# Performance work log

Hardware: AMD Instinct MI355X
Metric: run time of the kernel (lower is better)

The kernel has to match this reference:

```python
import jax, jax.numpy as jnp
import numpy as np

NUM_CLASSES = 10
THRESHOLD = 2e-4
ENT_COEF = 2e-4
COS_EPS = 1e-8
LOG_EPS = 1e-12


def setup_inputs() -> dict:
    key = jax.random.key(0)
    k1, k2, k3 = jax.random.split(key, 3)
    B, C, H, W = 256, 256, 8, 8
    M, F = 2000, C * H * W
    z = jax.random.normal(k1, (B, C, H, W), dtype=jnp.float32)
    labels = jax.random.randint(k2, (B,), 0, NUM_CLASSES)
    # kaiming-uniform-like init for the memory table
    bound = float(np.sqrt(6.0 / F))
    memory = jax.random.uniform(k3, (M, F), dtype=jnp.float32, minval=-bound, maxval=bound)
    return {"z": z, "labels": labels, "memory": memory}


def _shrink_l1norm(w):
    # hardshrink (strict |x| > lambda) then L1 renormalize along memories
    w = jnp.where(jnp.abs(w) > THRESHOLD, w, jnp.zeros_like(w))
    return w / jnp.sum(jnp.abs(w), axis=1, keepdims=True)


def _entropy_loss(w):
    return ENT_COEF * jnp.sum(-w * jnp.log(w + LOG_EPS))


def reference(z, labels, memory):
    B, C, H, W = z.shape
    M, F = memory.shape
    zf = z.reshape(B, F)
    # cosine similarity without materializing (B, M, F): dot / max(||z||*||m||, eps)
    nz = jnp.linalg.norm(zf, axis=1)              # (B,)
    nm = jnp.linalg.norm(memory, axis=1)          # (M,)
    logit = (zf @ memory.T) / jnp.maximum(nz[:, None] * nm[None, :], COS_EPS)  # (B, M)
    mem_weight = jax.nn.softmax(logit, axis=1)
    # per-class masks: memory slots are partitioned contiguously per class
    mem_per_class = M // NUM_CLASSES
    cls_of_mem = jnp.arange(M) // mem_per_class   # (M,)
    m1 = (cls_of_mem[None, :] == labels[:, None]).astype(mem_weight.dtype)  # target mask
    m2 = 1.0 - m1
    w_t = _shrink_l1norm(mem_weight * m1)
    w_nt = _shrink_l1norm(mem_weight * m2)
    z_hat_target = (w_t @ memory).reshape(B, C, H, W)
    z_hat_non_target = (w_nt @ memory).reshape(B, C, H, W)
    return (z_hat_target, z_hat_non_target, _entropy_loss(w_t), _entropy_loss(w_nt))
```

## Files before the change

kernel.cpp:

```cpp
#include <hip/hip_runtime.h>
#include <math.h>

#define BATCH 256
#define FDIM 16384
#define MSLOTS 2000
#define MPAD 2048
#define NCLS 10
#define MPC 200

static constexpr float THRESH = 2e-4f;
static constexpr float ENTC   = 2e-4f;
static constexpr float CEPS   = 1e-8f;
static constexpr float LEPS   = 1e-12f;

using bf16x8 = __attribute__((ext_vector_type(8))) short;
using f32x4  = __attribute__((ext_vector_type(4))) float;
using us8    = __attribute__((ext_vector_type(8))) unsigned short;

__device__ __forceinline__ unsigned short f2bf(float f) {
  unsigned u = __float_as_uint(f);
  unsigned r = u + 0x7fffu + ((u >> 16) & 1u);
  return (unsigned short)(r >> 16);
}

__device__ __forceinline__ void gload_lds16(const unsigned short* g, unsigned short* l) {
  __builtin_amdgcn_global_load_lds(
      (const __attribute__((address_space(1))) void*)g,
      (__attribute__((address_space(3))) void*)l, 16, 0, 0);
}

__device__ __forceinline__ float waveReduceSum(float v) {
#pragma unroll
  for (int o = 32; o > 0; o >>= 1) v += __shfl_xor(v, o);
  return v;
}
__device__ __forceinline__ float waveReduceMax(float v) {
#pragma unroll
  for (int o = 32; o > 0; o >>= 1) v = fmaxf(v, __shfl_xor(v, o));
  return v;
}


__global__ __launch_bounds__(256) void convert_z_kernel(const float* __restrict__ z,
                                                        unsigned short* __restrict__ zb,
                                                        float* __restrict__ nz) {
  const int b = blockIdx.x, tid = threadIdx.x;
  const float4* zr = reinterpret_cast<const float4*>(z + (size_t)b * FDIM);
  unsigned short* ob = zb + (size_t)b * FDIM;
  float s = 0.f;
  for (int i = tid; i < FDIM / 4; i += 256) {
    float4 v = zr[i];
    s = fmaf(v.x, v.x, fmaf(v.y, v.y, fmaf(v.z, v.z, fmaf(v.w, v.w, s))));
    ushort4 o;
    o.x = f2bf(v.x); o.y = f2bf(v.y); o.z = f2bf(v.z); o.w = f2bf(v.w);
    *reinterpret_cast<ushort4*>(&ob[i * 4]) = o;
  }
  s = waveReduceSum(s);
  __shared__ float red[4];
  if ((tid & 63) == 0) red[tid >> 6] = s;
  __syncthreads();
  if (tid == 0) nz[b] = sqrtf(red[0] + red[1] + red[2] + red[3]);
}

__global__ __launch_bounds__(256) void convert_mem_kernel(const float* __restrict__ mem,
                                                          unsigned short* __restrict__ mb,
                                                          float* __restrict__ nm) {
  const int r = blockIdx.x, tid = threadIdx.x;
  unsigned short* ob = mb + (size_t)r * FDIM;
  if (r >= MSLOTS) {
    us8 zed = (us8)0;
    for (int i = tid; i < FDIM / 8; i += 256)
      *reinterpret_cast<us8*>(&ob[i * 8]) = zed;
    if (tid == 0) nm[r] = 1.0f;
    return;
  }
  const float4* xr = reinterpret_cast<const float4*>(mem + (size_t)r * FDIM);
  float s = 0.f;
  for (int i = tid; i < FDIM / 4; i += 256) {
    float4 v = xr[i];
    s = fmaf(v.x, v.x, fmaf(v.y, v.y, fmaf(v.z, v.z, fmaf(v.w, v.w, s))));
    ushort4 o;
    o.x = f2bf(v.x); o.y = f2bf(v.y); o.z = f2bf(v.z); o.w = f2bf(v.w);
    *reinterpret_cast<ushort4*>(&ob[i * 4]) = o;
  }
  s = waveReduceSum(s);
  __shared__ float red[4];
  if ((tid & 63) == 0) red[tid >> 6] = s;
  __syncthreads();
  if (tid == 0) nm[r] = sqrtf(red[0] + red[1] + red[2] + red[3]);
}

__global__ __launch_bounds__(256) void transpose_kernel(const unsigned short* __restrict__ src,
                                                        unsigned short* __restrict__ dst) {
  __shared__ unsigned short t[64][72];
  const int f0 = blockIdx.x * 64, m0 = blockIdx.y * 64;
  const int tid = threadIdx.x;
#pragma unroll
  for (int it = 0; it < 2; ++it) {
    int r = (tid >> 3) + it * 32, c8 = tid & 7;
    us8 v = *reinterpret_cast<const us8*>(&src[(size_t)(m0 + r) * FDIM + f0 + c8 * 8]);
    *reinterpret_cast<us8*>(&t[r][c8 * 8]) = v;
  }
  __syncthreads();
#pragma unroll
  for (int it = 0; it < 2; ++it) {
    int rf = (tid >> 3) + it * 32, c8 = tid & 7;
    us8 v;
#pragma unroll
    for (int j = 0; j < 8; ++j) v[j] = t[c8 * 8 + j][rf];
    *reinterpret_cast<us8*>(&dst[(size_t)(f0 + rf) * MPAD + m0 + c8 * 8]) = v;
  }
}

#define G1_BM 128
#define G1_BN 64
#define G1_BK 64
#define SPLITK 8
#define KCHUNK (FDIM / SPLITK)

__global__ __launch_bounds__(256, 2) void gemm1_mfma(const unsigned short* __restrict__ zb,
                                                     const unsigned short* __restrict__ mb,
                                                     float* __restrict__ part) {
  __shared__ unsigned short As[G1_BM * G1_BK];
  __shared__ unsigned short Bs[G1_BN * G1_BK];
  const int tid = threadIdx.x;
  const int lane = tid & 63, wid = tid >> 6;
  const int bn0 = blockIdx.x * G1_BN;
  const int bm0 = blockIdx.y * G1_BM;
  const int kbase = blockIdx.z * KCHUNK;
  const int wr = wid >> 1, wc = wid & 1;
  const int l8 = lane >> 3, l7 = lane & 7;
  const int r16 = lane & 15, klane = lane >> 4;

  f32x4 acc[4][2] = {};

  for (int kt = 0; kt < KCHUNK; kt += G1_BK) {
    const int kg = kbase + kt;
#pragma unroll
    for (int it = 0; it < 4; ++it) {
      int c = wid + it * 4;
      int r = c * 8 + l8;
      int src = (l7 ^ (r & 7)) << 3;
      gload_lds16(&zb[(size_t)(bm0 + r) * FDIM + kg + src], &As[c * 512]);
    }
#pragma unroll
    for (int it = 0; it < 2; ++it) {
      int c = wid + it * 4;
      int r = c * 8 + l8;
      int src = (l7 ^ (r & 7)) << 3;
      gload_lds16(&mb[(size_t)(bn0 + r) * FDIM + kg + src], &Bs[c * 512]);
    }
    __syncthreads();
#pragma unroll
    for (int s = 0; s < 2; ++s) {
      bf16x8 a[4], bb[2];
#pragma unroll
      for (int i = 0; i < 4; ++i) {
        int r = wr * 64 + i * 16 + r16;
        int p = (s * 4 + klane) ^ (r & 7);
        a[i] = *reinterpret_cast<const bf16x8*>(&As[r * 64 + p * 8]);
      }
#pragma unroll
      for (int j = 0; j < 2; ++j) {
        int r = wc * 32 + j * 16 + r16;
        int p = (s * 4 + klane) ^ (r & 7);
        bb[j] = *reinterpret_cast<const bf16x8*>(&Bs[r * 64 + p * 8]);
      }
#pragma unroll
      for (int i = 0; i < 4; ++i)
#pragma unroll
        for (int j = 0; j < 2; ++j)
          acc[i][j] = __builtin_amdgcn_mfma_f32_16x16x32_bf16(a[i], bb[j], acc[i][j], 0, 0, 0);
    }
    __syncthreads();
  }
  const int rgrp = lane >> 4;
  float* pbase = part + (size_t)blockIdx.z * BATCH * MPAD;
#pragma unroll
  for (int i = 0; i < 4; ++i)
#pragma unroll
    for (int j = 0; j < 2; ++j)
#pragma unroll
      for (int rg = 0; rg < 4; ++rg) {
        int row = bm0 + wr * 64 + i * 16 + rgrp * 4 + rg;
        int col = bn0 + wc * 32 + j * 16 + r16;
        pbase[(size_t)row * MPAD + col] = acc[i][j][rg];
      }
}

__global__ __launch_bounds__(256) void softmax2_kernel(const float* __restrict__ part,
                                                       const float* __restrict__ nzv,
                                                       const float* __restrict__ nmv,
                                                       const int* __restrict__ labels,
                                                       unsigned short* __restrict__ wt,
                                                       unsigned short* __restrict__ wn,
                                                       float* __restrict__ ent) {
  const int b = blockIdx.x, tid = threadIdx.x;
  __shared__ float sh[MSLOTS];
  __shared__ float red[4], red2[4];
  const float nzb = nzv[b];
  float mx = -3.4e38f;
  for (int m = tid; m < MSLOTS; m += 256) {
    float s = 0.f;
#pragma unroll
    for (int sp = 0; sp < SPLITK; ++sp)
      s += part[((size_t)sp * BATCH + b) * MPAD + m];
    float v = s / fmaxf(nzb * nmv[m], CEPS);
    sh[m] = v; mx = fmaxf(mx, v);
  }
  mx = waveReduceMax(mx);
  if ((tid & 63) == 0) red[tid >> 6] = mx;
  __syncthreads();
  mx = fmaxf(fmaxf(red[0], red[1]), fmaxf(red[2], red[3]));
  __syncthreads();

  float s = 0.f;
  for (int m = tid; m < MSLOTS; m += 256) {
    float e = expf(sh[m] - mx); sh[m] = e; s += e;
  }
  s = waveReduceSum(s);
  if ((tid & 63) == 0) red[tid >> 6] = s;
  __syncthreads();
  s = red[0] + red[1] + red[2] + red[3];
  __syncthreads();

  const float inv = 1.f / s;
  const int c = labels[b];
  const int t0 = c * MPC, t1 = t0 + MPC;
  float st = 0.f, sn = 0.f;
  for (int m = tid; m < MSLOTS; m += 256) {
    float w = sh[m] * inv;
    float k = (w > THRESH) ? w : 0.f;
    sh[m] = k;
    bool tgt = (m >= t0) && (m < t1);
    st += tgt ? k : 0.f;
    sn += tgt ? 0.f : k;
  }
  st = waveReduceSum(st); sn = waveReduceSum(sn);
  if ((tid & 63) == 0) { red[tid >> 6] = st; red2[tid >> 6] = sn; }
  __syncthreads();
  st = red[0] + red[1] + red[2] + red[3];
  sn = red2[0] + red2[1] + red2[2] + red2[3];
  __syncthreads();

  const float rt = 1.f / st, rn = 1.f / sn;
  float et = 0.f, en = 0.f;
  unsigned short* wtr = wt + (size_t)b * MPAD;
  unsigned short* wnr = wn + (size_t)b * MPAD;
  for (int m = tid; m < MPAD; m += 256) {
    float a = 0.f, cn = 0.f;
    if (m < MSLOTS) {
      float k = sh[m];
      bool tgt = (m >= t0) && (m < t1);
      a  = tgt ? k * rt : 0.f;
      cn = tgt ? 0.f : k * rn;
      et -= a  * logf(a  + LEPS);
      en -= cn * logf(cn + LEPS);
    }
    wtr[m] = f2bf(a);
    wnr[m] = f2bf(cn);
  }
  et = waveReduceSum(et); en = waveReduceSum(en);
  if ((tid & 63) == 0) { red[tid >> 6] = et; red2[tid >> 6] = en; }
  __syncthreads();
  if (tid == 0) {
    ent[b]         = red[0] + red[1] + red[2] + red[3];
    ent[BATCH + b] = red2[0] + red2[1] + red2[2] + red2[3];
  }
}

#define G2_BM 128
#define G2_BN 128
#define G2_BK 64

__global__ __launch_bounds__(512, 2) void gemm23_mfma(const unsigned short* __restrict__ wt,
                                                      const unsigned short* __restrict__ wn,
                                                      const unsigned short* __restrict__ mt,
                                                      float* __restrict__ out) {
  __shared__ unsigned short At[G2_BM * G2_BK];
  __shared__ unsigned short An[G2_BM * G2_BK];
  __shared__ unsigned short Bs[G2_BN * G2_BK];
  const int tid = threadIdx.x, lane = tid & 63, wid = tid >> 6;
  const int bn0 = blockIdx.x * G2_BN;
  const int bm0 = blockIdx.y * G2_BM;
  const int wr = wid >> 2, wc = wid & 3;
  const int l8 = lane >> 3, l7 = lane & 7;
  const int r16 = lane & 15, klane = lane >> 4;

  f32x4 acct[4][2] = {}, accn[4][2] = {};

  for (int k0 = 0; k0 < MPAD; k0 += G2_BK) {
#pragma unroll
    for (int it = 0; it < 2; ++it) {
      int c = wid + it * 8;
      int r = c * 8 + l8;
      int src = (l7 ^ (r & 7)) << 3;
      gload_lds16(&wt[(size_t)(bm0 + r) * MPAD + k0 + src], &At[c * 512]);
      gload_lds16(&wn[(size_t)(bm0 + r) * MPAD + k0 + src], &An[c * 512]);
      gload_lds16(&mt[(size_t)(bn0 + r) * MPAD + k0 + src], &Bs[c * 512]);
    }
    __syncthreads();
#pragma unroll
    for (int s = 0; s < 2; ++s) {
      bf16x8 at[4], an[4], bb[2];
#pragma unroll
      for (int i = 0; i < 4; ++i) {
        int r = wr * 64 + i * 16 + r16;
        int p = (s * 4 + klane) ^ (r & 7);
        at[i] = *reinterpret_cast<const bf16x8*>(&At[r * 64 + p * 8]);
        an[i] = *reinterpret_cast<const bf16x8*>(&An[r * 64 + p * 8]);
      }
#pragma unroll
      for (int j = 0; j < 2; ++j) {
        int r = wc * 32 + j * 16 + r16;
        int p = (s * 4 + klane) ^ (r & 7);
        bb[j] = *reinterpret_cast<const bf16x8*>(&Bs[r * 64 + p * 8]);
      }
#pragma unroll
      for (int i = 0; i < 4; ++i)
#pragma unroll
        for (int j = 0; j < 2; ++j) {
          acct[i][j] = __builtin_amdgcn_mfma_f32_16x16x32_bf16(at[i], bb[j], acct[i][j], 0, 0, 0);
          accn[i][j] = __builtin_amdgcn_mfma_f32_16x16x32_bf16(an[i], bb[j], accn[i][j], 0, 0, 0);
        }
    }
    __syncthreads();
  }
  float* outn = out + (size_t)BATCH * FDIM;
  const int rgrp = lane >> 4;
#pragma unroll
  for (int i = 0; i < 4; ++i)
#pragma unroll
    for (int j = 0; j < 2; ++j)
#pragma unroll
      for (int rg = 0; rg < 4; ++rg) {
        size_t off = (size_t)(bm0 + wr * 64 + i * 16 + rgrp * 4 + rg) * FDIM
                   + bn0 + wc * 32 + j * 16 + r16;
        out[off]  = acct[i][j][rg];
        outn[off] = accn[i][j][rg];
      }
}

__global__ __launch_bounds__(256) void entreduce_kernel(const float* __restrict__ ent,
                                                        float* __restrict__ out) {
  const int tid = threadIdx.x;
  float v = ent[tid];
  float u = ent[BATCH + tid];
  v = waveReduceSum(v); u = waveReduceSum(u);
  __shared__ float r1[4], r2[4];
  if ((tid & 63) == 0) { r1[tid >> 6] = v; r2[tid >> 6] = u; }
  __syncthreads();
  if (tid == 0) {
    out[(size_t)2 * BATCH * FDIM]     = ENTC * (r1[0] + r1[1] + r1[2] + r1[3]);
    out[(size_t)2 * BATCH * FDIM + 1] = ENTC * (r2[0] + r2[1] + r2[2] + r2[3]);
  }
}

#define NM_OFF    0
#define NZ_OFF    2048
#define LOGIT_OFF 4096
#define WT_OFF    (LOGIT_OFF + 512000)
#define WNT_OFF   (WT_OFF + 512000)
#define ENT_OFF   (WNT_OFF + 512000)

__global__ __launch_bounds__(256) void rownorm_kernel(const float* __restrict__ x,
                                                      float* __restrict__ out, int cols) {
  const int r = blockIdx.x;
  const float4* xr = reinterpret_cast<const float4*>(x) + (size_t)r * (cols >> 2);
  const int n4 = cols >> 2;
  float s = 0.f;
  for (int i = threadIdx.x; i < n4; i += 256) {
    float4 v = xr[i];
    s = fmaf(v.x, v.x, s); s = fmaf(v.y, v.y, s);
    s = fmaf(v.z, v.z, s); s = fmaf(v.w, v.w, s);
  }
  s = waveReduceSum(s);
  __shared__ float red[4];
  if ((threadIdx.x & 63) == 0) red[threadIdx.x >> 6] = s;
  __syncthreads();
  if (threadIdx.x == 0) out[r] = sqrtf(red[0] + red[1] + red[2] + red[3]);
}

#define O1_BM 64
#define O1_BN 32
#define O1_BK 64
__global__ __launch_bounds__(256) void gemm1_kernel(const float* __restrict__ z,
                                                    const float* __restrict__ mem,
                                                    const float* __restrict__ nzv,
                                                    const float* __restrict__ nmv,
                                                    float* __restrict__ logit) {
  __shared__ float As[O1_BK][O1_BM];
  __shared__ float Bs[O1_BK][O1_BN];
  const int tid = threadIdx.x;
  const int bm0 = blockIdx.y * O1_BM;
  const int bn0 = blockIdx.x * O1_BN;
  const int tm = tid >> 4, tn = tid & 15;
  float acc[4][2] = {};
  for (int k0 = 0; k0 < FDIM; k0 += O1_BK) {
#pragma unroll
    for (int it = 0; it < 4; ++it) {
      int i = tid + it * 256;
      int row = i >> 4, c4 = i & 15;
      float4 v = *reinterpret_cast<const float4*>(&z[(size_t)(bm0 + row) * FDIM + k0 + c4 * 4]);
      As[c4 * 4 + 0][row] = v.x; As[c4 * 4 + 1][row] = v.y;
      As[c4 * 4 + 2][row] = v.z; As[c4 * 4 + 3][row] = v.w;
    }
#pragma unroll
    for (int it = 0; it < 2; ++it) {
      int i = tid + it * 256;
      int row = i >> 4, c4 = i & 15;
      int gm = bn0 + row;
      float4 v = make_float4(0.f, 0.f, 0.f, 0.f);
      if (gm < MSLOTS)
        v = *reinterpret_cast<const float4*>(&mem[(size_t)gm * FDIM + k0 + c4 * 4]);
      Bs[c4 * 4 + 0][row] = v.x; Bs[c4 * 4 + 1][row] = v.y;
      Bs[c4 * 4 + 2][row] = v.z; Bs[c4 * 4 + 3][row] = v.w;
    }
    __syncthreads();
#pragma unroll
    for (int kk = 0; kk < O1_BK; ++kk) {
      const float* ap = &As[kk][tm * 4];
      const float* bp = &Bs[kk][tn * 2];
      float a0 = ap[0], a1 = ap[1], a2 = ap[2], a3 = ap[3];
      float b0 = bp[0], b1 = bp[1];
      acc[0][0] = fmaf(a0, b0, acc[0][0]); acc[0][1] = fmaf(a0, b1, acc[0][1]);
      acc[1][0] = fmaf(a1, b0, acc[1][0]); acc[1][1] = fmaf(a1, b1, acc[1][1]);
      acc[2][0] = fmaf(a2, b0, acc[2][0]); acc[2][1] = fmaf(a2, b1, acc[2][1]);
      acc[3][0] = fmaf(a3, b0, acc[3][0]); acc[3][1] = fmaf(a3, b1, acc[3][1]);
    }
    __syncthreads();
  }
  float nzr[4];
#pragma unroll
  for (int i = 0; i < 4; ++i) nzr[i] = nzv[bm0 + tm * 4 + i];
#pragma unroll
  for (int j = 0; j < 2; ++j) {
    int col = bn0 + tn * 2 + j;
    if (col < MSLOTS) {
      float nmr = nmv[col];
#pragma unroll
      for (int i = 0; i < 4; ++i)
        logit[(size_t)(bm0 + tm * 4 + i) * MSLOTS + col] = acc[i][j] / fmaxf(nzr[i] * nmr, CEPS);
    }
  }
}

__global__ __launch_bounds__(256) void softmax_kernel(const float* __restrict__ logit,
                                                      const int* __restrict__ labels,
                                                      float* __restrict__ wt,
                                                      float* __restrict__ wnt,
                                                      float* __restrict__ ent) {
  const int b = blockIdx.x;
  const int tid = threadIdx.x;
  __shared__ float sh[MSLOTS];
  __shared__ float red[4], red2[4];
  const float* lrow = logit + (size_t)b * MSLOTS;
  float mx = -3.4e38f;
  for (int m = tid; m < MSLOTS; m += 256) {
    float v = lrow[m]; sh[m] = v; mx = fmaxf(mx, v);
  }
  mx = waveReduceMax(mx);
  if ((tid & 63) == 0) red[tid >> 6] = mx;
  __syncthreads();
  mx = fmaxf(fmaxf(red[0], red[1]), fmaxf(red[2], red[3]));
  __syncthreads();
  float s = 0.f;
  for (int m = tid; m < MSLOTS; m += 256) {
    float e = expf(sh[m] - mx); sh[m] = e; s += e;
  }
  s = waveReduceSum(s);
  if ((tid & 63) == 0) red[tid >> 6] = s;
  __syncthreads();
  s = red[0] + red[1] + red[2] + red[3];
  __syncthreads();
  const float inv = 1.f / s;
  const int c = labels[b];
  const int t0 = c * MPC, t1 = t0 + MPC;
  float st = 0.f, sn = 0.f;
  for (int m = tid; m < MSLOTS; m += 256) {
    float w = sh[m] * inv;
    float k = (w > THRESH) ? w : 0.f;
    sh[m] = k;
    bool tgt = (m >= t0) && (m < t1);
    st += tgt ? k : 0.f;
    sn += tgt ? 0.f : k;
  }
  st = waveReduceSum(st); sn = waveReduceSum(sn);
  if ((tid & 63) == 0) { red[tid >> 6] = st; red2[tid >> 6] = sn; }
  __syncthreads();
  st = red[0] + red[1] + red[2] + red[3];
  sn = red2[0] + red2[1] + red2[2] + red2[3];
  __syncthreads();
  const float rt = 1.f / st, rn = 1.f / sn;
  float et = 0.f, en = 0.f;
  float* wtr = wt + (size_t)b * MSLOTS;
  float* wnr = wnt + (size_t)b * MSLOTS;
  for (int m = tid; m < MSLOTS; m += 256) {
    float k = sh[m];
    bool tgt = (m >= t0) && (m < t1);
    float a  = tgt ? k * rt : 0.f;
    float cn = tgt ? 0.f : k * rn;
    wtr[m] = a;
    wnr[m] = cn;
    et -= a  * logf(a  + LEPS);
    en -= cn * logf(cn + LEPS);
  }
  et = waveReduceSum(et); en = waveReduceSum(en);
  if ((tid & 63) == 0) { red[tid >> 6] = et; red2[tid >> 6] = en; }
  __syncthreads();
  if (tid == 0) {
    ent[b]         = red[0] + red[1] + red[2] + red[3];
    ent[BATCH + b] = red2[0] + red2[1] + red2[2] + red2[3];
  }
}

#define O2_BM 64
#define O2_BN 64
#define O2_BK 32
__global__ __launch_bounds__(256) void gemm23_kernel(const float* __restrict__ wt,
                                                     const float* __restrict__ wnt,
                                                     const float* __restrict__ mem,
                                                     float* __restrict__ out) {
  __shared__ float Wts[O2_BK][O2_BM];
  __shared__ float Wns[O2_BK][O2_BM];
  __shared__ float Ms[O2_BK][O2_BN];
  const int tid = threadIdx.x;
  const int bm0 = blockIdx.y * O2_BM;
  const int bn0 = blockIdx.x * O2_BN;
  const int tm = tid >> 4, tn = tid & 15;
  float at[4][4] = {}, an[4][4] = {};
  for (int k0 = 0; k0 < MSLOTS; k0 += O2_BK) {
#pragma unroll
    for (int it = 0; it < 2; ++it) {
      int i = tid + it * 256;
      int row = i >> 3, c4 = i & 7;
      int gk = k0 + c4 * 4;
      float4 vt = make_float4(0.f, 0.f, 0.f, 0.f), vn = vt;
      if (gk < MSLOTS) {
        vt = *reinterpret_cast<const float4*>(&wt [(size_t)(bm0 + row) * MSLOTS + gk]);
        vn = *reinterpret_cast<const float4*>(&wnt[(size_t)(bm0 + row) * MSLOTS + gk]);
      }
      Wts[c4 * 4 + 0][row] = vt.x; Wts[c4 * 4 + 1][row] = vt.y;
      Wts[c4 * 4 + 2][row] = vt.z; Wts[c4 * 4 + 3][row] = vt.w;
      Wns[c4 * 4 + 0][row] = vn.x; Wns[c4 * 4 + 1][row] = vn.y;
      Wns[c4 * 4 + 2][row] = vn.z; Wns[c4 * 4 + 3][row] = vn.w;
    }
#pragma unroll
    for (int it = 0; it < 2; ++it) {
      int i = tid + it * 256;
      int row = i >> 4, c4 = i & 15;
      int gk = k0 + row;
      float4 v = make_float4(0.f, 0.f, 0.f, 0.f);
      if (gk < MSLOTS)
        v = *reinterpret_cast<const float4*>(&mem[(size_t)gk * FDIM + bn0 + c4 * 4]);
      *reinterpret_cast<float4*>(&Ms[row][c4 * 4]) = v;
    }
    __syncthreads();
#pragma unroll
    for (int kk = 0; kk < O2_BK; ++kk) {
      const float* tp = &Wts[kk][tm * 4];
      const float* np = &Wns[kk][tm * 4];
      const float* bp = &Ms[kk][tn * 4];
      float b0 = bp[0], b1 = bp[1], b2 = bp[2], b3 = bp[3];
#pragma unroll
      for (int i = 0; i < 4; ++i) {
        float a = tp[i], cn = np[i];
        at[i][0] = fmaf(a,  b0, at[i][0]); at[i][1] = fmaf(a,  b1, at[i][1]);
        at[i][2] = fmaf(a,  b2, at[i][2]); at[i][3] = fmaf(a,  b3, at[i][3]);
        an[i][0] = fmaf(cn, b0, an[i][0]); an[i][1] = fmaf(cn, b1, an[i][1]);
        an[i][2] = fmaf(cn, b2, an[i][2]); an[i][3] = fmaf(cn, b3, an[i][3]);
      }
    }
    __syncthreads();
  }
  float* outt = out;
  float* outn = out + (size_t)BATCH * FDIM;
#pragma unroll
  for (int i = 0; i < 4; ++i) {
    size_t off = (size_t)(bm0 + tm * 4 + i) * FDIM + bn0 + tn * 4;
    *reinterpret_cast<float4*>(&outt[off]) = make_float4(at[i][0], at[i][1], at[i][2], at[i][3]);
    *reinterpret_cast<float4*>(&outn[off]) = make_float4(an[i][0], an[i][1], an[i][2], an[i][3]);
  }
}

extern "C" void kernel_launch(void* const* d_in, const int* in_sizes, int n_in,
                              void* d_out, int out_size, void* d_ws, size_t ws_size,
                              hipStream_t stream) {
  const float* z      = (const float*)d_in[0];
  const int*   labels = (const int*)d_in[1];
  const float* mem    = (const float*)d_in[2];
  float* out = (float*)d_out;
  char*  wsb = (char*)d_ws;

  constexpr size_t NM_B  = 0;
  constexpr size_t NZ_B  = 8192;
  constexpr size_t ZB_B  = 16384;
  constexpr size_t MB_B  = ZB_B + (size_t)BATCH * FDIM * 2;
  constexpr size_t MT_B  = MB_B + (size_t)MPAD * FDIM * 2;
  constexpr size_t WTB_B = MT_B + (size_t)FDIM * MPAD * 2;
  constexpr size_t WNB_B = WTB_B + (size_t)BATCH * MPAD * 2;
  constexpr size_t PART_B = WNB_B + (size_t)BATCH * MPAD * 2;
  constexpr size_t ENT_B = PART_B + (size_t)SPLITK * BATCH * MPAD * 4;
  constexpr size_t NEED  = ENT_B + 2048;

  if (ws_size >= NEED) {
    float* nm = (float*)(wsb + NM_B);
    float* nz = (float*)(wsb + NZ_B);
    unsigned short* zb = (unsigned short*)(wsb + ZB_B);
    unsigned short* mb = (unsigned short*)(wsb + MB_B);
    unsigned short* mt = (unsigned short*)(wsb + MT_B);
    unsigned short* wt = (unsigned short*)(wsb + WTB_B);
    unsigned short* wn = (unsigned short*)(wsb + WNB_B);
    float* part = (float*)(wsb + PART_B);
    float* ent  = (float*)(wsb + ENT_B);

    convert_z_kernel<<<BATCH, 256, 0, stream>>>(z, zb, nz);
    convert_mem_kernel<<<MPAD, 256, 0, stream>>>(mem, mb, nm);
    transpose_kernel<<<dim3(FDIM / 64, MPAD / 64), 256, 0, stream>>>(mb, mt);
    gemm1_mfma<<<dim3(MPAD / G1_BN, BATCH / G1_BM, SPLITK), 256, 0, stream>>>(zb, mb, part);
    softmax2_kernel<<<BATCH, 256, 0, stream>>>(part, nz, nm, labels, wt, wn, ent);
    gemm23_mfma<<<dim3(FDIM / G2_BN, BATCH / G2_BM), 512, 0, stream>>>(wt, wn, mt, out);
    entreduce_kernel<<<1, 256, 0, stream>>>(ent, out);
  } else {
    float* ws    = (float*)d_ws;
    float* nm    = ws + NM_OFF;
    float* nzv   = ws + NZ_OFF;
    float* logit = ws + LOGIT_OFF;
    float* wt    = ws + WT_OFF;
    float* wnt   = ws + WNT_OFF;
    float* ent   = ws + ENT_OFF;

    rownorm_kernel<<<MSLOTS, 256, 0, stream>>>(mem, nm, FDIM);
    rownorm_kernel<<<BATCH, 256, 0, stream>>>(z, nzv, FDIM);
    gemm1_kernel<<<dim3((MSLOTS + O1_BN - 1) / O1_BN, BATCH / O1_BM), 256, 0, stream>>>(
        z, mem, nzv, nm, logit);
    softmax_kernel<<<BATCH, 256, 0, stream>>>(logit, labels, wt, wnt, ent);
    gemm23_kernel<<<dim3(FDIM / O2_BN, BATCH / O2_BM), 256, 0, stream>>>(wt, wnt, mem, out);
    entreduce_kernel<<<1, 256, 0, stream>>>(ent, out);
  }
}
```

Baseline: 168.5 us.

## Fuse bf16 conversion, row norms and transpose into one tiled kernel

Replaces the separate z/mem conversion kernels and the bf16 transpose kernel with a single 2D-tiled kernel. Each 64x64 tile is read from fp32, converted, and written as row-major bf16, and for memory tiles also transposed. Partial squared norms are written per tile and finished by a small reduction kernel. This avoids re-reading the bf16 memory copy for the transpose and cuts launches. In exchange, norms are now computed from bf16-rounded values and padding rows get a zero norm.

Measured after the change: 149.4 us. 1.13x faster.

```diff
diff --git a/kernel.cpp b/kernel.cpp
--- a/kernel.cpp
+++ b/kernel.cpp
@@ -7,6 +7,7 @@
 #define MPAD 2048
 #define NCLS 10
 #define MPC 200
+#define NFB (FDIM / 64)
 
 static constexpr float THRESH = 2e-4f;
 static constexpr float ENTC   = 2e-4f;
@@ -22,6 +23,9 @@
   unsigned r = u + 0x7fffu + ((u >> 16) & 1u);
   return (unsigned short)(r >> 16);
 }
+__device__ __forceinline__ float bf2f(unsigned short b) {
+  return __uint_as_float(((unsigned)b) << 16);
+}
 
 __device__ __forceinline__ void gload_lds16(const unsigned short* g, unsigned short* l) {
   __builtin_amdgcn_global_load_lds(
@@ -41,74 +45,83 @@
 }
 
 
-__global__ __launch_bounds__(256) void convert_z_kernel(const float* __restrict__ z,
-                                                        unsigned short* __restrict__ zb,
-                                                        float* __restrict__ nz) {
-  const int b = blockIdx.x, tid = threadIdx.x;
-  const float4* zr = reinterpret_cast<const float4*>(z + (size_t)b * FDIM);
-  unsigned short* ob = zb + (size_t)b * FDIM;
-  float s = 0.f;
-  for (int i = tid; i < FDIM / 4; i += 256) {
-    float4 v = zr[i];
-    s = fmaf(v.x, v.x, fmaf(v.y, v.y, fmaf(v.z, v.z, fmaf(v.w, v.w, s))));
+__global__ __launch_bounds__(256) void convert_all_kernel(
+    const float* __restrict__ z, const float* __restrict__ mem,
+    unsigned short* __restrict__ zb, unsigned short* __restrict__ mb,
+    unsigned short* __restrict__ mt, float* __restrict__ npart) {
+  __shared__ unsigned short t[64][72];
+  __shared__ float rsum[64][4];
+  const int tid = threadIdx.x;
+  const int f0 = blockIdx.x * 64;
+  const int yt = blockIdx.y;
+  const bool isMem = (yt < MPAD / 64);
+  const int r0 = isMem ? yt * 64 : (yt - MPAD / 64) * 64;
+  const float* src = isMem ? mem : z;
+
+#pragma unroll
+  for (int it = 0; it < 4; ++it) {
+    int i = tid + it * 256;
+    int r = i >> 4, c4 = i & 15;
+    int gr = r0 + r;
+    float4 v = make_float4(0.f, 0.f, 0.f, 0.f);
+    if (!isMem || gr < MSLOTS)
+      v = *reinterpret_cast<const float4*>(&src[(size_t)gr * FDIM + f0 + c4 * 4]);
     ushort4 o;
     o.x = f2bf(v.x); o.y = f2bf(v.y); o.z = f2bf(v.z); o.w = f2bf(v.w);
-    *reinterpret_cast<ushort4*>(&ob[i * 4]) = o;
-  }
+    *reinterpret_cast<ushort4*>(&t[r][c4 * 4]) = o;
+  }
+  __syncthreads();
+  {
+    int r = tid & 63, q = tid >> 6;
+    float s = 0.f;
+#pragma unroll
+    for (int c = 0; c < 16; ++c) {
+      float val = bf2f(t[r][q * 16 + c]);
+      s = fmaf(val, val, s);
+    }
+    rsum[r][q] = s;
+  }
+  __syncthreads();
+  if (tid < 64) {
+    float s = rsum[tid][0] + rsum[tid][1] + rsum[tid][2] + rsum[tid][3];
+    int row = isMem ? (r0 + tid) : (MPAD + r0 + tid);
+    npart[(size_t)row * NFB + blockIdx.x] = s;
+  }
+  unsigned short* dst = isMem ? mb : zb;
+#pragma unroll
+  for (int it = 0; it < 2; ++it) {
+    int i = tid + it * 256;
+    int r = i >> 3, c8 = i & 7;
+    us8 v = *reinterpret_cast<const us8*>(&t[r][c8 * 8]);
+    *reinterpret_cast<us8*>(&dst[(size_t)(r0 + r) * FDIM + f0 + c8 * 8]) = v;
+  }
+  if (isMem) {
+#pragma unroll
+    for (int it = 0; it < 2; ++it) {
+      int i = tid + it * 256;
+      int fr = i >> 3, c8 = i & 7;
+      us8 v;
+#pragma unroll
+      for (int j = 0; j < 8; ++j) v[j] = t[c8 * 8 + j][fr];
+      *reinterpret_cast<us8*>(&mt[(size_t)(f0 + fr) * MPAD + r0 + c8 * 8]) = v;
+    }
+  }
+}
+
+__global__ __launch_bounds__(64) void normfin_kernel(const float* __restrict__ npart,
+                                                     float* __restrict__ nm,
+                                                     float* __restrict__ nz) {
+  const int row = blockIdx.x;
+  const int lane = threadIdx.x;
+  const float* p = npart + (size_t)row * NFB;
+  float s = 0.f;
+#pragma unroll
+  for (int k = 0; k < NFB / 64; ++k) s += p[lane + k * 64];
   s = waveReduceSum(s);
-  __shared__ float red[4];
-  if ((tid & 63) == 0) red[tid >> 6] = s;
-  __syncthreads();
-  if (tid == 0) nz[b] = sqrtf(red[0] + red[1] + red[2] + red[3]);
-}
-
-__global__ __launch_bounds__(256) void convert_mem_kernel(const float* __restrict__ mem,
-                                                          unsigned short* __restrict__ mb,
-                                                          float* __restrict__ nm) {
-  const int r = blockIdx.x, tid = threadIdx.x;
-  unsigned short* ob = mb + (size_t)r * FDIM;
-  if (r >= MSLOTS) {
-    us8 zed = (us8)0;
-    for (int i = tid; i < FDIM / 8; i += 256)
-      *reinterpret_cast<us8*>(&ob[i * 8]) = zed;
-    if (tid == 0) nm[r] = 1.0f;
-    return;
-  }
-  const float4* xr = reinterpret_cast<const float4*>(mem + (size_t)r * FDIM);
-  float s = 0.f;
-  for (int i = tid; i < FDIM / 4; i += 256) {
-    float4 v = xr[i];
-    s = fmaf(v.x, v.x, fmaf(v.y, v.y, fmaf(v.z, v.z, fmaf(v.w, v.w, s))));
-    ushort4 o;
-    o.x = f2bf(v.x); o.y = f2bf(v.y); o.z = f2bf(v.z); o.w = f2bf(v.w);
-    *reinterpret_cast<ushort4*>(&ob[i * 4]) = o;
-  }
-  s = waveReduceSum(s);
-  __shared__ float red[4];
-  if ((tid & 63) == 0) red[tid >> 6] = s;
-  __syncthreads();
-  if (tid == 0) nm[r] = sqrtf(red[0] + red[1] + red[2] + red[3]);
-}
-
-__global__ __launch_bounds__(256) void transpose_kernel(const unsigned short* __restrict__ src,
-                                                        unsigned short* __restrict__ dst) {
-  __shared__ unsigned short t[64][72];
-  const int f0 = blockIdx.x * 64, m0 = blockIdx.y * 64;
-  const int tid = threadIdx.x;
-#pragma unroll
-  for (int it = 0; it < 2; ++it) {
-    int r = (tid >> 3) + it * 32, c8 = tid & 7;
-    us8 v = *reinterpret_cast<const us8*>(&src[(size_t)(m0 + r) * FDIM + f0 + c8 * 8]);
-    *reinterpret_cast<us8*>(&t[r][c8 * 8]) = v;
-  }
-  __syncthreads();
-#pragma unroll
-  for (int it = 0; it < 2; ++it) {
-    int rf = (tid >> 3) + it * 32, c8 = tid & 7;
-    us8 v;
-#pragma unroll
-    for (int j = 0; j < 8; ++j) v[j] = t[c8 * 8 + j][rf];
-    *reinterpret_cast<us8*>(&dst[(size_t)(f0 + rf) * MPAD + m0 + c8 * 8]) = v;
+  if (lane == 0) {
+    float v = sqrtf(s);
+    if (row < MPAD) nm[row] = v;
+    else            nz[row - MPAD] = v;
   }
 }
 
@@ -592,16 +605,17 @@
   float* out = (float*)d_out;
   char*  wsb = (char*)d_ws;
 
-  constexpr size_t NM_B  = 0;
-  constexpr size_t NZ_B  = 8192;
-  constexpr size_t ZB_B  = 16384;
-  constexpr size_t MB_B  = ZB_B + (size_t)BATCH * FDIM * 2;
-  constexpr size_t MT_B  = MB_B + (size_t)MPAD * FDIM * 2;
-  constexpr size_t WTB_B = MT_B + (size_t)FDIM * MPAD * 2;
-  constexpr size_t WNB_B = WTB_B + (size_t)BATCH * MPAD * 2;
-  constexpr size_t PART_B = WNB_B + (size_t)BATCH * MPAD * 2;
-  constexpr size_t ENT_B = PART_B + (size_t)SPLITK * BATCH * MPAD * 4;
-  constexpr size_t NEED  = ENT_B + 2048;
+  constexpr size_t NM_B   = 0;
+  constexpr size_t NZ_B   = 8192;
+  constexpr size_t ZB_B   = 16384;
+  constexpr size_t MB_B   = ZB_B + (size_t)BATCH * FDIM * 2;
+  constexpr size_t MT_B   = MB_B + (size_t)MPAD * FDIM * 2;
+  constexpr size_t WTB_B  = MT_B + (size_t)FDIM * MPAD * 2;
+  constexpr size_t WNB_B  = WTB_B + (size_t)BATCH * MPAD * 2;
+  constexpr size_t NP_B   = WNB_B + (size_t)BATCH * MPAD * 2;
+  constexpr size_t PART_B = NP_B + (size_t)(MPAD + BATCH) * NFB * 4;
+  constexpr size_t ENT_B  = PART_B + (size_t)SPLITK * BATCH * MPAD * 4;
+  constexpr size_t NEED   = ENT_B + 2048;
 
   if (ws_size >= NEED) {
     float* nm = (float*)(wsb + NM_B);
@@ -611,12 +625,13 @@
     unsigned short* mt = (unsigned short*)(wsb + MT_B);
     unsigned short* wt = (unsigned short*)(wsb + WTB_B);
     unsigned short* wn = (unsigned short*)(wsb + WNB_B);
-    float* part = (float*)(wsb + PART_B);
-    float* ent  = (float*)(wsb + ENT_B);
-
-    convert_z_kernel<<<BATCH, 256, 0, stream>>>(z, zb, nz);
-    convert_mem_kernel<<<MPAD, 256, 0, stream>>>(mem, mb, nm);
-    transpose_kernel<<<dim3(FDIM / 64, MPAD / 64), 256, 0, stream>>>(mb, mt);
+    float* npart = (float*)(wsb + NP_B);
+    float* part  = (float*)(wsb + PART_B);
+    float* ent   = (float*)(wsb + ENT_B);
+
+    convert_all_kernel<<<dim3(NFB, (MPAD + BATCH) / 64), 256, 0, stream>>>(
+        z, mem, zb, mb, mt, npart);
+    normfin_kernel<<<MPAD + BATCH, 64, 0, stream>>>(npart, nm, nz);
     gemm1_mfma<<<dim3(MPAD / G1_BN, BATCH / G1_BM, SPLITK), 256, 0, stream>>>(zb, mb, part);
     softmax2_kernel<<<BATCH, 256, 0, stream>>>(part, nz, nm, labels, wt, wn, ent);
     gemm23_mfma<<<dim3(FDIM / G2_BN, BATCH / G2_BM), 512, 0, stream>>>(wt, wn, mt, out);
```
